# Kernel tuning notes

Measured on AMD Instinct MI355X. Metric: run time of the kernel, lower is better.

The kernel has to match this reference:

```python
import jax, jax.numpy as jnp
import numpy as np

P = 17  # prediction chunk size
H = 50  # hidden size

def _lstm_cell(x, h, c, Wih, Whh, bih, bhh):
    # torch LSTMCell: gates = x@Wih^T + bih + h@Whh^T + bhh, order i,f,g,o
    g = x @ Wih.T + h @ Whh.T + (bih + bhh)
    i, f, gg, o = jnp.split(g, 4, axis=-1)
    c_new = jax.nn.sigmoid(f) * c + jax.nn.sigmoid(i) * jnp.tanh(gg)
    h_new = jax.nn.sigmoid(o) * jnp.tanh(c_new)
    return h_new, c_new

def setup_inputs() -> dict:
    key = jax.random.key(0)
    ks = jax.random.split(key, 16)
    B, T = 2048, 512
    s = 1.0 / np.sqrt(H)
    u = lambda k, shp: jax.random.uniform(k, shp, jnp.float32, -s, s)
    return {
        "x": jax.random.normal(ks[0], (B, T * P), jnp.float32),
        "W_ih1": u(ks[1], (4 * H, P)),  "W_hh1": u(ks[2], (4 * H, H)),
        "b_ih1": u(ks[3], (4 * H,)),    "b_hh1": u(ks[4], (4 * H,)),
        "W_ih2": u(ks[5], (4 * H, H)),  "W_hh2": u(ks[6], (4 * H, H)),
        "b_ih2": u(ks[7], (4 * H,)),    "b_hh2": u(ks[8], (4 * H,)),
        "W_ih3": u(ks[9], (4 * H, H)),  "W_hh3": u(ks[10], (4 * H, H)),
        "b_ih3": u(ks[11], (4 * H,)),   "b_hh3": u(ks[12], (4 * H,)),
        "W_lin": u(ks[13], (P, H)),     "b_lin": u(ks[14], (P,)),
        "future": 544,
    }

def reference(x, W_ih1, W_hh1, b_ih1, b_hh1, W_ih2, W_hh2, b_ih2, b_hh2,
              W_ih3, W_hh3, b_ih3, b_hh3, W_lin, b_lin, future):
    B = x.shape[0]
    T = x.shape[1] // P
    xs = x.reshape(B, T, P).transpose(1, 0, 2)  # [T, B, P]
    z = jnp.zeros((B, H), jnp.float32)
    init = (z, z, z, z, z, z)

    def cell_stack(state, inp):
        h1, c1, h2, c2, h3, c3 = state
        h1, c1 = _lstm_cell(inp, h1, c1, W_ih1, W_hh1, b_ih1, b_hh1)
        h2, c2 = _lstm_cell(h1, h2, c2, W_ih2, W_hh2, b_ih2, b_hh2)
        h3, c3 = _lstm_cell(h2, h3, c3, W_ih3, W_hh3, b_ih3, b_hh3)
        out = h3 @ W_lin.T + b_lin  # [B, P]
        return (h1, c1, h2, c2, h3, c3), out

    def step(state, xt):
        return cell_stack(state, xt)

    state, outs = jax.lax.scan(step, init, xs)  # outs: [T, B, P]

    n_future = int(future) // P
    if n_future > 0:
        last = outs[-1]

        def fstep(carry, _):
            state, out = carry
            state, out = cell_stack(state, out)
            return (state, out), out

        _, fouts = jax.lax.scan(fstep, (state, last), None, length=n_future)
        outs = jnp.concatenate([outs, fouts], axis=0)  # [T+next, B, P]

    return outs.transpose(1, 0, 2).reshape(B, -1)  # [B, (T+next)*P]
```

## Files before the change

kernel.cpp:

```cpp
#include <hip/hip_runtime.h>
#include <math.h>


#define BATCH    2048
#define PP       17
#define HH       50
#define GG       200
#define MROWS    8
#define NTHREADS 512
#define NBLOCKS  (BATCH / MROWS)

__device__ __forceinline__ float bf2f(unsigned short u) {
    unsigned int i = ((unsigned int)u) << 16;
    float f; __builtin_memcpy(&f, &i, 4); return f;
}
__device__ __forceinline__ unsigned short f2bf(float f) {
    unsigned int i; __builtin_memcpy(&i, &f, 4);
    return (unsigned short)((i + 0x7fffu + ((i >> 16) & 1u)) >> 16);
}
__device__ __forceinline__ float ldin(const void* p, long i, bool f32) {
    return f32 ? ((const float*)p)[i] : bf2f(((const unsigned short*)p)[i]);
}
__device__ __forceinline__ float fsig(float x) {
    float t = exp2f(-1.44269504089f * x);
    return __builtin_amdgcn_rcpf(1.0f + t);
}
__device__ __forceinline__ float ftanh(float x) {
    float t = exp2f(2.88539008178f * x);
    return 1.0f - 2.0f * __builtin_amdgcn_rcpf(t + 1.0f);
}

extern "C" __global__ void sniff_dtype(const unsigned short* __restrict__ w,
                                       int* __restrict__ flag) {
    int lane = threadIdx.x;
    bool bad = false;
#pragma unroll
    for (int t = 0; t < 4; ++t) {
        float v = bf2f(w[lane * 4 + t]);
        bad |= !(fabsf(v) <= 1.0f);
    }
    unsigned long long m = __ballot(bad);
    if (lane == 0) flag[0] = (m != 0ULL) ? 1 : 0;
}

template <int TQ>
__device__ __forceinline__ void gate_phase(const float* __restrict__ S,
                                           float* __restrict__ gb,
                                           const float w[2][TQ],
                                           int srow, int g2, int q, bool active) {
    if (active) {
        float aA[8] = {0, 0, 0, 0, 0, 0, 0, 0};
        float aB[8] = {0, 0, 0, 0, 0, 0, 0, 0};
        const float4* Sp = (const float4*)(S + (srow + q * TQ) * MROWS);
#pragma unroll
        for (int t = 0; t < TQ; ++t) {
            float wa = w[0][t], wb = w[1][t];
            float4 lo = Sp[2 * t];
            float4 hi = Sp[2 * t + 1];
            aA[0] = fmaf(wa, lo.x, aA[0]); aA[1] = fmaf(wa, lo.y, aA[1]);
            aA[2] = fmaf(wa, lo.z, aA[2]); aA[3] = fmaf(wa, lo.w, aA[3]);
            aA[4] = fmaf(wa, hi.x, aA[4]); aA[5] = fmaf(wa, hi.y, aA[5]);
            aA[6] = fmaf(wa, hi.z, aA[6]); aA[7] = fmaf(wa, hi.w, aA[7]);
            aB[0] = fmaf(wb, lo.x, aB[0]); aB[1] = fmaf(wb, lo.y, aB[1]);
            aB[2] = fmaf(wb, lo.z, aB[2]); aB[3] = fmaf(wb, lo.w, aB[3]);
            aB[4] = fmaf(wb, hi.x, aB[4]); aB[5] = fmaf(wb, hi.y, aB[5]);
            aB[6] = fmaf(wb, hi.z, aB[6]); aB[7] = fmaf(wb, hi.w, aB[7]);
        }
#pragma unroll
        for (int m = 0; m < 8; ++m) {
            float2 v; v.x = aA[m]; v.y = aB[m];
            ((float2*)(gb + (q * MROWS + m) * GG))[g2] = v;
        }
    }
}

__device__ __forceinline__ void lstm_update(float* __restrict__ S,
                                            const float* __restrict__ gb,
                                            const float* __restrict__ bs,
                                            float& c, int hrow, int tid) {
    int m = tid & 7;
    int j = tid >> 3;
    float ii = bs[j], ff = bs[50 + j], gg = bs[100 + j], oo = bs[150 + j];
#pragma unroll
    for (int q = 0; q < 4; ++q) {
        const float* b = gb + (q * MROWS + m) * GG;
        ii += b[j]; ff += b[50 + j]; gg += b[100 + j]; oo += b[150 + j];
    }
    float cn = fsig(ff) * c + fsig(ii) * ftanh(gg);
    c = cn;
    S[(hrow + j) * MROWS + m] = fsig(oo) * ftanh(cn);
}

extern "C" __global__ void __launch_bounds__(NTHREADS, 2)
lstm_persistent(const void* __restrict__ x,
                const void* __restrict__ wih1, const void* __restrict__ whh1,
                const void* __restrict__ bih1, const void* __restrict__ bhh1,
                const void* __restrict__ wih2, const void* __restrict__ whh2,
                const void* __restrict__ bih2, const void* __restrict__ bhh2,
                const void* __restrict__ wih3, const void* __restrict__ whh3,
                const void* __restrict__ bih3, const void* __restrict__ bhh3,
                const void* __restrict__ wlin, const void* __restrict__ blin,
                void* __restrict__ out, const int* __restrict__ flag,
                int T, int steps)
{
    const int tid = threadIdx.x;
    __shared__ float S[167 * MROWS];
    __shared__ float gb[4 * MROWS * GG];
    __shared__ float WLt[50 * PP];
    __shared__ float bs1[GG], bs2[GG], bs3[GG], bl[PP];

    const bool f32 = (flag[0] != 0);

    const int q  = tid >> 7;
    const int g2 = tid & 127;
    const bool active = (g2 < 100);

    float w1[2][17], w2[2][25], w3[2][25];
    if (active) {
#pragma unroll
        for (int e = 0; e < 2; ++e) {
            const int g = 2 * g2 + e;
#pragma unroll
            for (int t = 0; t < 17; ++t) {
                int k = q * 17 + t;
                w1[e][t] = (k < 17) ? ldin(wih1, (long)g * 17 + k, f32)
                         : (k < 67) ? ldin(whh1, (long)g * 50 + (k - 17), f32)
                                    : 0.0f;
            }
#pragma unroll
            for (int t = 0; t < 25; ++t) {
                int k = q * 25 + t;
                w2[e][t] = (k < 50) ? ldin(wih2, (long)g * 50 + k, f32)
                                    : ldin(whh2, (long)g * 50 + (k - 50), f32);
            }
#pragma unroll
            for (int t = 0; t < 25; ++t) {
                int k = q * 25 + t;
                w3[e][t] = (k < 50) ? ldin(wih3, (long)g * 50 + k, f32)
                                    : ldin(whh3, (long)g * 50 + (k - 50), f32);
            }
        }
    }

    if (tid < GG) {
        bs1[tid] = ldin(bih1, tid, f32) + ldin(bhh1, tid, f32);
        bs2[tid] = ldin(bih2, tid, f32) + ldin(bhh2, tid, f32);
        bs3[tid] = ldin(bih3, tid, f32) + ldin(bhh3, tid, f32);
    } else if (tid < GG + PP) {
        bl[tid - GG] = ldin(blin, tid - GG, f32);
    }
    for (int i = tid; i < 50 * PP; i += NTHREADS) {
        int k = i / PP, p = i - k * PP;
        WLt[i] = ldin(wlin, (long)p * 50 + k, f32);
    }
    for (int i = tid; i < 1200; i += NTHREADS) S[136 + i] = 0.0f;

    const long rowBase = (long)blockIdx.x * MROWS;
    const long xStride = (long)T * PP;
    if (tid < 136) {
        int m = tid / PP, p = tid - (tid / PP) * PP;
        S[p * MROWS + m] = ldin(x, (rowBase + m) * xStride + p, f32);
    }
    float c1 = 0.0f, c2 = 0.0f, c3 = 0.0f;
    __syncthreads();

    const long outStride = (long)steps * PP;
    for (int s = 0; s < steps; ++s) {
        gate_phase<17>(S, gb, w1, 0, g2, q, active);
        __syncthreads();
        if (tid < 400) lstm_update(S, gb, bs1, c1, 17, tid);
        __syncthreads();
        gate_phase<25>(S, gb, w2, 17, g2, q, active);
        __syncthreads();
        if (tid < 400) lstm_update(S, gb, bs2, c2, 67, tid);
        __syncthreads();
        gate_phase<25>(S, gb, w3, 67, g2, q, active);
        __syncthreads();
        if (tid < 400) lstm_update(S, gb, bs3, c3, 117, tid);
        __syncthreads();
        if (tid < 136) {
            int m = tid / PP, p = tid - (tid / PP) * PP;
            float acc = bl[p];
#pragma unroll
            for (int k = 0; k < 50; ++k)
                acc = fmaf(WLt[k * PP + p], S[(117 + k) * MROWS + m], acc);
            long oi = (rowBase + m) * outStride + (long)s * PP + p;
            if (f32) ((float*)out)[oi] = acc;
            else     ((unsigned short*)out)[oi] = f2bf(acc);
            if (s + 1 >= T && s + 1 < steps)
                S[p * MROWS + m] = acc;
        } else if (tid >= 256 && tid < 392) {
            int u = tid - 256;
            int m = u / PP, p = u - (u / PP) * PP;
            if (s + 1 < T)
                S[p * MROWS + m] = ldin(x, (rowBase + m) * xStride + (long)(s + 1) * PP + p, f32);
        }
        __syncthreads();
    }
}

extern "C" void kernel_launch(void* const* d_in, const int* in_sizes, int n_in,
                              void* d_out, int out_size, void* d_ws, size_t ws_size,
                              hipStream_t stream) {
    (void)ws_size; (void)n_in;
    int* flag = (int*)d_ws;

    const int T     = in_sizes[0] / (BATCH * PP);
    const int steps = out_size / (BATCH * PP);

    sniff_dtype<<<1, 64, 0, stream>>>((const unsigned short*)d_in[1], flag);

    lstm_persistent<<<NBLOCKS, NTHREADS, 0, stream>>>(
        d_in[0],
        d_in[1], d_in[2], d_in[3], d_in[4],
        d_in[5], d_in[6], d_in[7], d_in[8],
        d_in[9], d_in[10], d_in[11], d_in[12],
        d_in[13], d_in[14],
        d_out, flag, T, steps);
}
```

Baseline: 3.808 ms.

## Split gate reduction into 8 K-slices with float4 gate packing and prefetch x

```diff
diff --git a/kernel.cpp b/kernel.cpp
--- a/kernel.cpp
+++ b/kernel.cpp
@@ -9,6 +9,10 @@
 #define MROWS    8
 #define NTHREADS 512
 #define NBLOCKS  (BATCH / MROWS)
+#define KQ1      9
+#define KQ2      13
+#define KQ3      13
+#define SROWS    171
 
 __device__ __forceinline__ float bf2f(unsigned short u) {
     unsigned int i = ((unsigned int)u) << 16;
@@ -45,53 +49,54 @@
 
 template <int TQ>
 __device__ __forceinline__ void gate_phase(const float* __restrict__ S,
-                                           float* __restrict__ gb,
-                                           const float w[2][TQ],
-                                           int srow, int g2, int q, bool active) {
-    if (active) {
-        float aA[8] = {0, 0, 0, 0, 0, 0, 0, 0};
-        float aB[8] = {0, 0, 0, 0, 0, 0, 0, 0};
-        const float4* Sp = (const float4*)(S + (srow + q * TQ) * MROWS);
-#pragma unroll
-        for (int t = 0; t < TQ; ++t) {
-            float wa = w[0][t], wb = w[1][t];
-            float4 lo = Sp[2 * t];
-            float4 hi = Sp[2 * t + 1];
-            aA[0] = fmaf(wa, lo.x, aA[0]); aA[1] = fmaf(wa, lo.y, aA[1]);
-            aA[2] = fmaf(wa, lo.z, aA[2]); aA[3] = fmaf(wa, lo.w, aA[3]);
-            aA[4] = fmaf(wa, hi.x, aA[4]); aA[5] = fmaf(wa, hi.y, aA[5]);
-            aA[6] = fmaf(wa, hi.z, aA[6]); aA[7] = fmaf(wa, hi.w, aA[7]);
-            aB[0] = fmaf(wb, lo.x, aB[0]); aB[1] = fmaf(wb, lo.y, aB[1]);
-            aB[2] = fmaf(wb, lo.z, aB[2]); aB[3] = fmaf(wb, lo.w, aB[3]);
-            aB[4] = fmaf(wb, hi.x, aB[4]); aB[5] = fmaf(wb, hi.y, aB[5]);
-            aB[6] = fmaf(wb, hi.z, aB[6]); aB[7] = fmaf(wb, hi.w, aB[7]);
-        }
-#pragma unroll
-        for (int m = 0; m < 8; ++m) {
-            float2 v; v.x = aA[m]; v.y = aB[m];
-            ((float2*)(gb + (q * MROWS + m) * GG))[g2] = v;
-        }
+                                           float4* __restrict__ gb4,
+                                           const float (&w)[4][TQ],
+                                           int srow, int g4, int q, bool act) {
+    if (!act) return;
+    float a[4][8];
+#pragma unroll
+    for (int e = 0; e < 4; ++e)
+#pragma unroll
+        for (int m = 0; m < 8; ++m) a[e][m] = 0.0f;
+    const float4* Sp = (const float4*)(S + (srow + q * TQ) * MROWS);
+#pragma unroll
+    for (int t = 0; t < TQ; ++t) {
+        float4 lo = Sp[2 * t];
+        float4 hi = Sp[2 * t + 1];
+#pragma unroll
+        for (int e = 0; e < 4; ++e) {
+            float wv = w[e][t];
+            a[e][0] = fmaf(wv, lo.x, a[e][0]); a[e][1] = fmaf(wv, lo.y, a[e][1]);
+            a[e][2] = fmaf(wv, lo.z, a[e][2]); a[e][3] = fmaf(wv, lo.w, a[e][3]);
+            a[e][4] = fmaf(wv, hi.x, a[e][4]); a[e][5] = fmaf(wv, hi.y, a[e][5]);
+            a[e][6] = fmaf(wv, hi.z, a[e][6]); a[e][7] = fmaf(wv, hi.w, a[e][7]);
+        }
+    }
+#pragma unroll
+    for (int m = 0; m < 8; ++m) {
+        float4 v; v.x = a[0][m]; v.y = a[1][m]; v.z = a[2][m]; v.w = a[3][m];
+        gb4[(q * MROWS + m) * HH + g4] = v;
     }
 }
 
 __device__ __forceinline__ void lstm_update(float* __restrict__ S,
-                                            const float* __restrict__ gb,
-                                            const float* __restrict__ bs,
+                                            const float4* __restrict__ gb4,
+                                            const float4* __restrict__ bsv,
                                             float& c, int hrow, int tid) {
     int m = tid & 7;
     int j = tid >> 3;
-    float ii = bs[j], ff = bs[50 + j], gg = bs[100 + j], oo = bs[150 + j];
-#pragma unroll
-    for (int q = 0; q < 4; ++q) {
-        const float* b = gb + (q * MROWS + m) * GG;
-        ii += b[j]; ff += b[50 + j]; gg += b[100 + j]; oo += b[150 + j];
-    }
-    float cn = fsig(ff) * c + fsig(ii) * ftanh(gg);
+    float4 s = bsv[j];
+#pragma unroll
+    for (int q = 0; q < 8; ++q) {
+        float4 v = gb4[(q * MROWS + m) * HH + j];
+        s.x += v.x; s.y += v.y; s.z += v.z; s.w += v.w;
+    }
+    float cn = fsig(s.y) * c + fsig(s.x) * ftanh(s.z);
     c = cn;
-    S[(hrow + j) * MROWS + m] = fsig(oo) * ftanh(cn);
-}
-
-extern "C" __global__ void __launch_bounds__(NTHREADS, 2)
+    S[(hrow + j) * MROWS + m] = fsig(s.w) * ftanh(cn);
+}
+
+extern "C" __global__ void __launch_bounds__(NTHREADS, 1)
 lstm_persistent(const void* __restrict__ x,
                 const void* __restrict__ wih1, const void* __restrict__ whh1,
                 const void* __restrict__ bih1, const void* __restrict__ bhh1,
@@ -104,56 +109,66 @@
                 int T, int steps)
 {
     const int tid = threadIdx.x;
-    __shared__ float S[167 * MROWS];
-    __shared__ float gb[4 * MROWS * GG];
-    __shared__ float WLt[50 * PP];
-    __shared__ float bs1[GG], bs2[GG], bs3[GG], bl[PP];
+    __shared__ float  S[SROWS * MROWS];
+    __shared__ float4 gb4[8 * MROWS * HH];
+    __shared__ float4 bsv[3][HH];
+    __shared__ float  WLt[PP][52];
+    __shared__ float  bl[PP];
 
     const bool f32 = (flag[0] != 0);
 
-    const int q  = tid >> 7;
-    const int g2 = tid & 127;
-    const bool active = (g2 < 100);
-
-    float w1[2][17], w2[2][25], w3[2][25];
-    if (active) {
-#pragma unroll
-        for (int e = 0; e < 2; ++e) {
-            const int g = 2 * g2 + e;
-#pragma unroll
-            for (int t = 0; t < 17; ++t) {
-                int k = q * 17 + t;
+    const int lane = tid & 63;
+    const int q    = tid >> 6;
+    const int g4   = lane;
+    const bool act = (lane < HH);
+
+    float w1[4][KQ1], w2[4][KQ2], w3[4][KQ3];
+    if (act) {
+#pragma unroll
+        for (int e = 0; e < 4; ++e) {
+            const int g = e * HH + g4;
+#pragma unroll
+            for (int t = 0; t < KQ1; ++t) {
+                int k = q * KQ1 + t;
                 w1[e][t] = (k < 17) ? ldin(wih1, (long)g * 17 + k, f32)
                          : (k < 67) ? ldin(whh1, (long)g * 50 + (k - 17), f32)
                                     : 0.0f;
             }
 #pragma unroll
-            for (int t = 0; t < 25; ++t) {
-                int k = q * 25 + t;
-                w2[e][t] = (k < 50) ? ldin(wih2, (long)g * 50 + k, f32)
-                                    : ldin(whh2, (long)g * 50 + (k - 50), f32);
-            }
-#pragma unroll
-            for (int t = 0; t < 25; ++t) {
-                int k = q * 25 + t;
-                w3[e][t] = (k < 50) ? ldin(wih3, (long)g * 50 + k, f32)
-                                    : ldin(whh3, (long)g * 50 + (k - 50), f32);
-            }
-        }
-    }
-
-    if (tid < GG) {
-        bs1[tid] = ldin(bih1, tid, f32) + ldin(bhh1, tid, f32);
-        bs2[tid] = ldin(bih2, tid, f32) + ldin(bhh2, tid, f32);
-        bs3[tid] = ldin(bih3, tid, f32) + ldin(bhh3, tid, f32);
-    } else if (tid < GG + PP) {
-        bl[tid - GG] = ldin(blin, tid - GG, f32);
-    }
-    for (int i = tid; i < 50 * PP; i += NTHREADS) {
-        int k = i / PP, p = i - k * PP;
-        WLt[i] = ldin(wlin, (long)p * 50 + k, f32);
-    }
-    for (int i = tid; i < 1200; i += NTHREADS) S[136 + i] = 0.0f;
+            for (int t = 0; t < KQ2; ++t) {
+                int k = q * KQ2 + t;
+                w2[e][t] = (k < 50)  ? ldin(wih2, (long)g * 50 + k, f32)
+                         : (k < 100) ? ldin(whh2, (long)g * 50 + (k - 50), f32)
+                                     : 0.0f;
+            }
+#pragma unroll
+            for (int t = 0; t < KQ3; ++t) {
+                int k = q * KQ3 + t;
+                w3[e][t] = (k < 50)  ? ldin(wih3, (long)g * 50 + k, f32)
+                         : (k < 100) ? ldin(whh3, (long)g * 50 + (k - 50), f32)
+                                     : 0.0f;
+            }
+        }
+    }
+
+    if (tid < 150) {
+        int cc = tid / HH, j = tid - cc * HH;
+        const void* bi = (cc == 0) ? bih1 : (cc == 1) ? bih2 : bih3;
+        const void* bh = (cc == 0) ? bhh1 : (cc == 1) ? bhh2 : bhh3;
+        float4 v;
+        v.x = ldin(bi, j,       f32) + ldin(bh, j,       f32);
+        v.y = ldin(bi, 50 + j,  f32) + ldin(bh, 50 + j,  f32);
+        v.z = ldin(bi, 100 + j, f32) + ldin(bh, 100 + j, f32);
+        v.w = ldin(bi, 150 + j, f32) + ldin(bh, 150 + j, f32);
+        bsv[cc][j] = v;
+    } else if (tid < 150 + PP) {
+        bl[tid - 150] = ldin(blin, tid - 150, f32);
+    }
+    for (int i = tid; i < PP * 52; i += NTHREADS) {
+        int p = i / 52, k = i - p * 52;
+        WLt[p][k] = (k < 50) ? ldin(wlin, (long)p * 50 + k, f32) : 0.0f;
+    }
+    for (int i = tid; i < SROWS * MROWS - 136; i += NTHREADS) S[136 + i] = 0.0f;
 
     const long rowBase = (long)blockIdx.x * MROWS;
     const long xStride = (long)T * PP;
@@ -166,34 +181,51 @@
 
     const long outStride = (long)steps * PP;
     for (int s = 0; s < steps; ++s) {
-        gate_phase<17>(S, gb, w1, 0, g2, q, active);
-        __syncthreads();
-        if (tid < 400) lstm_update(S, gb, bs1, c1, 17, tid);
-        __syncthreads();
-        gate_phase<25>(S, gb, w2, 17, g2, q, active);
-        __syncthreads();
-        if (tid < 400) lstm_update(S, gb, bs2, c2, 67, tid);
-        __syncthreads();
-        gate_phase<25>(S, gb, w3, 67, g2, q, active);
-        __syncthreads();
-        if (tid < 400) lstm_update(S, gb, bs3, c3, 117, tid);
+        float xp0 = 0.0f, xp1 = 0.0f;
+        int u0 = 136, u1 = 136;
+        if (lane >= HH && s + 1 < T) {
+            int idx = q * 14 + (lane - HH);
+            u0 = idx; u1 = idx + 112;
+            if (u0 < 136)
+                xp0 = ldin(x, (rowBase + u0 / PP) * xStride + (long)(s + 1) * PP + (u0 % PP), f32);
+            if (u1 < 136)
+                xp1 = ldin(x, (rowBase + u1 / PP) * xStride + (long)(s + 1) * PP + (u1 % PP), f32);
+        }
+
+        gate_phase<KQ1>(S, gb4, w1, 0, g4, q, act);
+        __syncthreads();
+        if (tid < 400) lstm_update(S, gb4, bsv[0], c1, 17, tid);
+        __syncthreads();
+        gate_phase<KQ2>(S, gb4, w2, 17, g4, q, act);
+        __syncthreads();
+        if (tid < 400) lstm_update(S, gb4, bsv[1], c2, 67, tid);
+        __syncthreads();
+        gate_phase<KQ3>(S, gb4, w3, 67, g4, q, act);
+        __syncthreads();
+        if (tid < 400) lstm_update(S, gb4, bsv[2], c3, 117, tid);
         __syncthreads();
         if (tid < 136) {
             int m = tid / PP, p = tid - (tid / PP) * PP;
             float acc = bl[p];
-#pragma unroll
-            for (int k = 0; k < 50; ++k)
-                acc = fmaf(WLt[k * PP + p], S[(117 + k) * MROWS + m], acc);
+            const float4* wp = (const float4*)(&WLt[p][0]);
+#pragma unroll
+            for (int kk = 0; kk < 13; ++kk) {
+                float4 wv = wp[kk];
+                int k = 4 * kk;
+                acc = fmaf(wv.x, S[(117 + k) * MROWS + m], acc);
+                acc = fmaf(wv.y, S[(118 + k) * MROWS + m], acc);
+                acc = fmaf(wv.z, S[(119 + k) * MROWS + m], acc);
+                acc = fmaf(wv.w, S[(120 + k) * MROWS + m], acc);
+            }
             long oi = (rowBase + m) * outStride + (long)s * PP + p;
             if (f32) ((float*)out)[oi] = acc;
             else     ((unsigned short*)out)[oi] = f2bf(acc);
             if (s + 1 >= T && s + 1 < steps)
                 S[p * MROWS + m] = acc;
-        } else if (tid >= 256 && tid < 392) {
-            int u = tid - 256;
-            int m = u / PP, p = u - (u / PP) * PP;
-            if (s + 1 < T)
-                S[p * MROWS + m] = ldin(x, (rowBase + m) * xStride + (long)(s + 1) * PP + p, f32);
+        }
+        if (lane >= HH && s + 1 < T) {
+            if (u0 < 136) S[(u0 % PP) * MROWS + (u0 / PP)] = xp0;
+            if (u1 < 136) S[(u1 % PP) * MROWS + (u1 / PP)] = xp1;
         }
         __syncthreads();
     }
```

New measurement: 4.572 ms. +20.1%, slower.
